# Optimization experiments

Measured on AMD Instinct MI355X. Metric: run time of the kernel, lower is better.

The kernel has to match this reference:

```python
import jax, jax.numpy as jnp
import numpy as np
from jax import lax

# problem sizes and solver hyperparameters
B, N, G, T = 8, 128, 100, 24
N_ITERS, LR, RHO = 40, 2e-4, 10.0
VOLL, VOSP = 1000.0, 50.0
RES_UP, RES_DN, RT_UP, RT_DN, RAMP_F = 0.05, 0.02, 2.0, 0.5, 1.0


def setup_inputs() -> dict:
    k = jax.random.split(jax.random.key(0), 8)
    pmin = jax.random.uniform(k[0], (G,), minval=10.0, maxval=50.0)
    pmax = pmin + jax.random.uniform(k[1], (G,), minval=100.0, maxval=300.0)
    b_G = jax.random.uniform(k[2], (G,), minval=10.0, maxval=40.0)
    c_G = jax.random.uniform(k[3], (G,), minval=0.0, maxval=5.0)
    lo, hi = pmin.sum(), pmax.sum()
    forecast = lo + jax.random.uniform(k[4], (B, T)) * 0.5 * (hi - lo)
    omega_scen = 0.05 * hi * jax.random.normal(k[5], (B, N, T))
    om_min = omega_scen.min(axis=1) - 1.0
    om_max = omega_scen.max(axis=1) + 1.0
    eps = jax.random.uniform(k[6], (B,)) * 5.0
    return dict(forecast=forecast, omega_scen=omega_scen, om_min=om_min,
                om_max=om_max, eps=eps, pmin=pmin, pmax=pmax, b_G=b_G, c_G=c_G)


def _solve_one(forecast, omega, om_min, om_max, eps, pmin, pmax, b, c):
    # forecast [T], omega [N,T], om_min/om_max [T], eps scalar
    ramp = pmax * RAMP_F
    rup_p, rdn_p = RES_UP * b, RES_DN * b
    rtu_p, rtd_p = RT_UP * b, RT_DN * b
    dist_max = (om_max[None, :] - omega).sum(-1)   # [N]
    dist_min = (omega - om_min[None, :]).sum(-1)   # [N]

    def objective(v):
        Cost = b[:, None] * v['P'] + c[:, None]
        stage1 = (Cost.sum() + (rup_p[:, None] * v['R_up']).sum()
                  + (rdn_p[:, None] * v['R_dn']).sum())
        Qn = (jnp.einsum('g,ngt->n', rtu_p, v['d_up'])
              + jnp.einsum('g,ngt->n', rtd_p, v['d_dn'])
              + VOLL * v['LS'].sum(-1) + VOSP * v['SP'].sum(-1))
        Qmax = ((rtu_p[:, None] * v['du_max']).sum() + (rtd_p[:, None] * v['dd_max']).sum()
                + VOLL * v['LS_max'].sum() + VOSP * v['SP_max'].sum())
        Qmin = ((rtu_p[:, None] * v['du_min']).sum() + (rtd_p[:, None] * v['dd_min']).sum()
                + VOLL * v['LS_min'].sum() + VOSP * v['SP_min'].sum())
        # epigraph phi[n] >= Qn, >= Qmax - gamma*dist_max, >= Qmin - gamma*dist_min
        phi = jnp.maximum(Qn, jnp.maximum(Qmax - v['gamma'] * dist_max,
                                          Qmin - v['gamma'] * dist_min))
        obj = stage1 + phi.mean() + eps * v['gamma']
        return obj, (phi, Cost)

    def penalty(v):
        relu = jax.nn.relu
        dP = v['P'][:, 1:] - v['P'][:, :-1]
        res = [
            # equality constraints
            v['P'].sum(0) - forecast,
            (v['d_up'] - v['d_dn']).sum(1) + v['LS'] - v['SP'] - omega,
            (v['du_max'] - v['dd_max']).sum(0) + v['LS_max'] - v['SP_max'] - om_max,
            (v['du_min'] - v['dd_min']).sum(0) + v['LS_min'] - v['SP_min'] - om_min,
            # inequality constraints (relu of violation)
            relu(v['P'] + v['R_up'] - pmax[:, None]),
            relu(pmin[:, None] - (v['P'] - v['R_dn'])),
            relu(v['d_up'] - v['R_up'][None]),
            relu(v['d_dn'] - v['R_dn'][None]),
            relu(v['du_max'] - v['R_up']), relu(v['dd_max'] - v['R_dn']),
            relu(v['du_min'] - v['R_up']), relu(v['dd_min'] - v['R_dn']),
            relu(jnp.abs(dP) - ramp[:, None]),
        ]
        total = jnp.zeros(())
        for r in res:
            total = total + (r * r).sum()
        return total

    def loss(v):
        return objective(v)[0] + RHO * penalty(v)

    def project(v):
        v = {kk: jnp.maximum(vv, 0.0) for kk, vv in v.items()}
        v['P'] = jnp.clip(v['P'], pmin[:, None], pmax[:, None])
        return v

    z_gt = jnp.zeros((G, T))
    v0 = {'P': jnp.broadcast_to(0.5 * (pmin + pmax)[:, None], (G, T)),
          'R_up': z_gt, 'R_dn': z_gt,
          'd_up': jnp.zeros((N, G, T)), 'd_dn': jnp.zeros((N, G, T)),
          'LS': jnp.zeros((N, T)), 'SP': jnp.zeros((N, T)),
          'du_max': z_gt, 'dd_max': z_gt,
          'LS_max': jnp.zeros((T,)), 'SP_max': jnp.zeros((T,)),
          'du_min': z_gt, 'dd_min': z_gt,
          'LS_min': jnp.zeros((T,)), 'SP_min': jnp.zeros((T,)),
          'gamma': jnp.zeros(())}
    grad_fn = jax.grad(loss)

    def step(v, _):
        g = grad_fn(v)
        v = jax.tree_util.tree_map(lambda x, gx: x - LR * gx, v, g)
        return project(v), None

    v, _ = lax.scan(step, v0, None, length=N_ITERS)
    obj, (phi, Cost) = objective(v)
    return v['P'], v['R_up'], v['R_dn'], Cost, phi, v['gamma'], obj


def reference(forecast, omega_scen, om_min, om_max, eps, pmin, pmax, b_G, c_G):
    solve = jax.vmap(_solve_one, in_axes=(0, 0, 0, 0, 0, None, None, None, None))
    P, R_up, R_dn, Cost, phi, gamma, obj = solve(
        forecast, omega_scen, om_min, om_max, eps, pmin, pmax, b_G, c_G)
    return P, R_up, R_dn, Cost, phi, gamma, obj
```

## Files before the change

### kernel.cpp

```cpp
#include <hip/hip_runtime.h>
#include <hip/hip_cooperative_groups.h>

namespace cg = cooperative_groups;

#define G_ 100
#define T_ 24
#define NSC 128
#define BATCH 8
#define NITER 40
#define NBLK (BATCH*T_)
#define NTHR 512
#define GMAX 13

typedef unsigned long long u64;

__device__ __forceinline__ u64 gload64(const u64* p){
  return __hip_atomic_load(p, __ATOMIC_RELAXED, __HIP_MEMORY_SCOPE_AGENT);
}
__device__ __forceinline__ void gstore64(u64* p, u64 v){
  __hip_atomic_store(p, v, __ATOMIC_RELAXED, __HIP_MEMORY_SCOPE_AGENT);
}
__device__ __forceinline__ u64 pack(float v, unsigned tag){
  return ((u64)tag<<32) | (u64)__float_as_uint(v);
}
__device__ __forceinline__ float unpackv(u64 x){ return __uint_as_float((unsigned)x); }
__device__ __forceinline__ unsigned unpackt(u64 x){ return (unsigned)(x>>32); }

__device__ __forceinline__ void blockReduce2(float& a, float& b, float* sR){
#pragma unroll
  for (int off=32; off; off>>=1){ a+=__shfl_down(a,off,64); b+=__shfl_down(b,off,64); }
  const int w = threadIdx.x>>6;
  __syncthreads();
  if ((threadIdx.x&63)==0){ sR[w]=a; sR[8+w]=b; }
  __syncthreads();
  a=0.f; b=0.f;
#pragma unroll
  for (int i=0;i<8;++i){ a+=sR[i]; b+=sR[8+i]; }
}

__global__ __launch_bounds__(NTHR, 1) void dro_kernel(
    const float* __restrict__ forecast, const float* __restrict__ omega,
    const float* __restrict__ om_min, const float* __restrict__ om_max,
    const float* __restrict__ eps_in, const float* __restrict__ pmin_g,
    const float* __restrict__ pmax_g, const float* __restrict__ bG,
    const float* __restrict__ cG, float* __restrict__ out, float* __restrict__ ws)
{
  constexpr float LR=2e-4f, VOLL=1000.f, VOSP=50.f, TWO_RHO=20.f, INVN=1.f/128.f;
  const int blk=blockIdx.x;
  const int b=blk&7;
  const int t_own=blk>>3;
  const int tid=threadIdx.x, wave=tid>>6, lane=tid&63;
  const int gcnt  = (wave<4)? 13 : 12;
  const int gbase = (wave<4)? wave*13 : 52+(wave-4)*12;

  __shared__ float sRu[G_], sRd[G_];
  __shared__ float sP[G_], sduM[G_], sddM[G_], sdum[G_], sddm[G_];
  __shared__ float sAccU[G_], sAccD[G_];
  __shared__ float sB[G_], sPmin[G_], sPmax[G_], sC[G_];
  __shared__ float sLS[NSC], sSP[NSC], sOm[NSC];
  __shared__ float sGQ[NSC], sR220[NSC];
  __shared__ float sQn[NSC], sDM[NSC], sDm[NSC], sS2[NSC];
  __shared__ float sQp[NSC*9], sSp[NSC*9];
  __shared__ float sQnP[NTHR];
  __shared__ float sRed[40];
  __shared__ float sScal[12];

  u64* W = (u64*)ws;
  u64* QNP = W;
  u64* PP  = W + 73728;
  u64* QS  = W + 147456;
  u64* GAM = W + 156672;
  u64* ST1 = W + 157056;

  const float epsv  = eps_in[b];
  const float omaxT = om_max[b*T_ + t_own];
  const float ominT = om_min[b*T_ + t_own];
  const float fctT  = forecast[b*T_ + t_own];

  float duA[GMAX], duB[GMAX], ddA[GMAX], ddB[GMAX];

  if (tid<G_){
    sB[tid]=bG[tid]; sPmin[tid]=pmin_g[tid]; sPmax[tid]=pmax_g[tid]; sC[tid]=cG[tid];
    sRu[tid]=0.f; sRd[tid]=0.f;
    sduM[tid]=0.f; sddM[tid]=0.f; sdum[tid]=0.f; sddm[tid]=0.f;
    sAccU[tid]=0.f; sAccD[tid]=0.f;
  }
  if (tid<NSC){
    const int n=tid;
    sLS[n]=0.f; sSP[n]=0.f; sS2[n]=0.f;
    sOm[n]=omega[(b*NSC+n)*T_+t_own];
    float dM=0.f,dm=0.f;
    for (int t=0;t<T_;++t){
      float o=omega[(b*NSC+n)*T_+t];
      dM+=om_max[b*T_+t]-o; dm+=o-om_min[b*T_+t];
    }
    sDM[n]=dM; sDm[n]=dm;
  }
  if (tid==0){ sScal[3]=0.f; sScal[4]=0.f; sScal[5]=0.f; sScal[6]=0.f; }
  __syncthreads();
#pragma unroll
  for (int j=0;j<GMAX;++j){ duA[j]=0.f; duB[j]=0.f; ddA[j]=0.f; ddB[j]=0.f; }
  {
    float p0=0.f;
    if (tid<G_){
      p0=0.5f*(sPmin[tid]+sPmax[tid]);
      sP[tid]=p0;
      gstore64(&PP[b*3072 + t_own*128 + tid], pack(p0,1u));
    }
    if (tid<NSC) gstore64(&QNP[b*3072 + t_own*128 + tid], pack(0.f,1u));
    if (tid<2)   gstore64(&QS[(b*T_ + t_own)*16 + tid], pack(0.f,1u));
    if (t_own==0 && tid==0) gstore64(&GAM[b*16], pack(0.f,1u));
    float rp=p0, dum0=0.f;
    blockReduce2(rp,dum0,sRed);
    if (tid==0){
      sScal[0]=-omaxT; sScal[1]=-ominT; sScal[2]=rp-fctT;
    }
  }
  __syncthreads();

  for (int k=0;k<=NITER;++k){
    const unsigned tg = (unsigned)(k+1);
    const int rb = k%3, wb = (k+1)%3;
    const u64* qnpR = QNP + rb*24576 + b*3072;
    const u64* ppR  = PP  + rb*24576 + b*3072;
    const u64* qsR  = QS  + (rb*BATCH + b)*T_*16;
    const u64* gamR = GAM + (rb*BATCH + b)*16;
    u64* qnpW = QNP + wb*24576 + b*3072 + t_own*128;
    u64* ppW  = PP  + wb*24576 + b*3072 + t_own*128;
    u64* qsW  = QS  + (wb*BATCH + b)*T_*16 + t_own*16;
    u64* gamW = GAM + (wb*BATCH + b)*16;

    const int n = tid&127, sb0 = (tid>>7)*6;
    u64 xq[6];
#pragma unroll
    for (int s=0;s<6;++s) xq[s]=gload64(&qnpR[(sb0+s)*128 + n]);
    u64 xm=0, xp=0;
    if (tid<G_){
      if (t_own>0)     xm = gload64(&ppR[(t_own-1)*128 + tid]);
      if (t_own<T_-1)  xp = gload64(&ppR[(t_own+1)*128 + tid]);
    }
    u64 xs0=0, xs1=0, xg=0;
    if (wave==0){
      if (lane<T_){ xs0=gload64(&qsR[lane*16]); xs1=gload64(&qsR[lane*16+1]); }
      xg=gload64(gamR);
    }
    for (;;){
      bool any=false;
#pragma unroll
      for (int s=0;s<6;++s)
        if (unpackt(xq[s])!=tg){ any=true; xq[s]=gload64(&qnpR[(sb0+s)*128 + n]); }
      if (!any) break;
      __builtin_amdgcn_s_sleep(1);
    }
    if (tid<G_){
      if (t_own>0)    while (unpackt(xm)!=tg){ __builtin_amdgcn_s_sleep(1); xm=gload64(&ppR[(t_own-1)*128 + tid]); }
      if (t_own<T_-1) while (unpackt(xp)!=tg){ __builtin_amdgcn_s_sleep(1); xp=gload64(&ppR[(t_own+1)*128 + tid]); }
    }
    float Qmax=0.f, Qmin=0.f, gamma=0.f;
    if (wave==0){
      if (lane<T_){
        while (unpackt(xs0)!=tg){ __builtin_amdgcn_s_sleep(1); xs0=gload64(&qsR[lane*16]); }
        while (unpackt(xs1)!=tg){ __builtin_amdgcn_s_sleep(1); xs1=gload64(&qsR[lane*16+1]); }
        Qmax=unpackv(xs0); Qmin=unpackv(xs1);
      }
      while (unpackt(xg)!=tg){ __builtin_amdgcn_s_sleep(1); xg=gload64(gamR); }
      gamma=unpackv(xg);
      if (lane==0) sScal[11]=gamma;
    }
    sQnP[tid]=unpackv(xq[0])+unpackv(xq[1])+unpackv(xq[2])
             +unpackv(xq[3])+unpackv(xq[4])+unpackv(xq[5]);
    const float pm1=unpackv(xm), pp1=unpackv(xp);
    __syncthreads();

    if (k==NITER){
      if (wave==0){
#pragma unroll
        for (int off=32; off; off>>=1){ Qmax+=__shfl_xor(Qmax,off,64); Qmin+=__shfl_xor(Qmin,off,64); }
        if (lane==0){ sScal[8]=Qmax; sScal[9]=Qmin; }
      }
      __syncthreads();
      const float Qm=sScal[8], Qn2=sScal[9], gam=sScal[11];
      if (tid<NSC){
        const float qsum=sQnP[tid]+sQnP[tid+128]+sQnP[tid+256]+sQnP[tid+384];
        const float ph=fmaxf(qsum,fmaxf(Qm-gam*sDM[tid],Qn2-gam*sDm[tid]));
        sQn[tid]=ph;
        if (t_own==0) out[76800 + b*NSC + tid]=ph;
      }
      float st=0.f, dum0=0.f;
      if (tid<G_){
        const int g=tid;
        const float Pv=sP[g];
        const float costv=sB[g]*Pv+sC[g];
        st=costv + 0.05f*sB[g]*sRu[g] + 0.02f*sB[g]*sRd[g];
        const int o=b*2400 + g*T_ + t_own;
        out[o]=Pv;
        out[19200+o]=sRu[g];
        out[38400+o]=sRd[g];
        out[57600+o]=costv;
      }
      blockReduce2(st,dum0,sRed);
      if (tid==0) gstore64(&ST1[(b*T_+t_own)*16], pack(st,99u));
      if (t_own==0){
        if (tid==0) out[77824+b]=gam;
        float s1=0.f;
        if (tid<64){
          u64 xs = (lane<T_)? gload64(&ST1[(b*T_+lane)*16]) : pack(0.f,99u);
          while (unpackt(xs)!=99u){ __builtin_amdgcn_s_sleep(1); xs=gload64(&ST1[(b*T_+lane)*16]); }
          s1=unpackv(xs);
        }
        float pm=(tid<NSC)? sQn[tid] : 0.f;
        blockReduce2(pm,s1,sRed);
        if (tid==0) out[77832+b] = s1 + pm*INVN + epsv*gam;
      }
      break;
    }

    if (wave==0){
#pragma unroll
      for (int off=32; off; off>>=1){ Qmax+=__shfl_xor(Qmax,off,64); Qmin+=__shfl_xor(Qmin,off,64); }
      float g1l=0.f,g2l=0.f,sgl=0.f;
#pragma unroll
      for (int h=0;h<2;++h){
        const int nn=lane+h*64;
        const float Qn=sQnP[nn]+sQnP[nn+128]+sQnP[nn+256]+sQnP[nn+384];
        const float m1=Qmax-gamma*sDM[nn], m2=Qmin-gamma*sDm[nn];
        const float inner=fmaxf(m1,m2), ph=fmaxf(Qn,inner);
        const float gQn=(Qn==ph?1.f:0.f)/((inner==ph)?2.f:1.f);
        const float gIn=(inner==ph?1.f:0.f)/((Qn==ph)?2.f:1.f);
        const float gm1=gIn*(m1==inner?1.f:0.f)/((m2==inner)?2.f:1.f);
        const float gm2=gIn*(m2==inner?1.f:0.f)/((m1==inner)?2.f:1.f);
        const float gq=gQn*INVN;
        sGQ[nn]=gq;
        g1l+=gm1; g2l+=gm2; sgl+=gm1*sDM[nn]+gm2*sDm[nn];
        const float r2=sS2[nn]+sLS[nn]-sSP[nn]-sOm[nn];
        const float r220=TWO_RHO*r2;
        sR220[nn]=r220;
        sLS[nn]=fmaxf(sLS[nn]-LR*(gq*VOLL+r220),0.f);
        sSP[nn]=fmaxf(sSP[nn]-LR*(gq*VOSP-r220),0.f);
      }
#pragma unroll
      for (int off=32; off; off>>=1){
        g1l+=__shfl_xor(g1l,off,64); g2l+=__shfl_xor(g2l,off,64); sgl+=__shfl_xor(sgl,off,64);
      }
      if (lane==0){ sScal[8]=g1l; sScal[9]=g2l; sScal[10]=sgl; }
    }
    __syncthreads();

    const float gqA=sGQ[lane],    r220A=sR220[lane];
    const float gqB=sGQ[lane+64], r220B=sR220[lane+64];
    float qvA=0.f,qvB=0.f,svA=0.f,svB=0.f;
#pragma unroll
    for (int j=0;j<GMAX;++j){
      if (j<gcnt){
        const int g=gbase+j;
        const float bg=sB[g];
        const float rtu=2.f*bg, rtd=0.5f*bg;
        const float ru=sRu[g], rd=sRd[g];
        const float r7A=fmaxf(duA[j]-ru,0.f), r8A=fmaxf(ddA[j]-rd,0.f);
        const float r7B=fmaxf(duB[j]-ru,0.f), r8B=fmaxf(ddB[j]-rd,0.f);
        duA[j]=fmaxf(duA[j]-LR*(gqA*rtu+(r220A+TWO_RHO*r7A)),0.f);
        ddA[j]=fmaxf(ddA[j]-LR*(gqA*rtd+(TWO_RHO*r8A-r220A)),0.f);
        duB[j]=fmaxf(duB[j]-LR*(gqB*rtu+(r220B+TWO_RHO*r7B)),0.f);
        ddB[j]=fmaxf(ddB[j]-LR*(gqB*rtd+(TWO_RHO*r8B-r220B)),0.f);
        qvA+=rtu*duA[j]+rtd*ddA[j];  svA+=duA[j]-ddA[j];
        qvB+=rtu*duB[j]+rtd*ddB[j];  svB+=duB[j]-ddB[j];
      }
    }
    sQp[lane*9+wave]=qvA;      sSp[lane*9+wave]=svA;
    sQp[(lane+64)*9+wave]=qvB; sSp[(lane+64)*9+wave]=svB;
    __syncthreads();

    const unsigned tg2 = (unsigned)(k+2);
    if (tid>=256 && tid<384){
      const int nn=tid-256;
      float q=0.f,s=0.f;
#pragma unroll
      for (int w=0;w<8;++w){ q+=sQp[nn*9+w]; s+=sSp[nn*9+w]; }
      sS2[nn]=s;
      q += VOLL*sLS[nn]+VOSP*sSP[nn];
      gstore64(&qnpW[nn], pack(q,tg2));
    }
    const float r3=sScal[0], r4=sScal[1], rP=sScal[2];
    const float S1s=sScal[8], S2s=sScal[9];
    float pQx=0.f,pQn2=0.f,pr3=0.f,pr4=0.f,pP=0.f;
    if (tid<G_){
      const int g=tid;
      const float rupS=sAccU[g], rdnS=sAccD[g];
      const float Pold=sP[g], ru=sRu[g], rd=sRd[g];
      const float duMo=sduM[g], ddMo=sddM[g], dumo=sdum[g], ddmo=sddm[g];
      const float r5 =fmaxf(Pold+ru-sPmax[g],0.f);
      const float r6 =fmaxf(sPmin[g]-Pold+rd,0.f);
      const float r9 =fmaxf(duMo-ru,0.f), r10=fmaxf(ddMo-rd,0.f);
      const float r11=fmaxf(dumo-ru,0.f), r12=fmaxf(ddmo-rd,0.f);
      const float rampg=sPmax[g];
      float gP=sB[g]+TWO_RHO*(rP+r5-r6);
      if (t_own>0){
        const float dp=Pold-pm1;
        gP+=TWO_RHO*fmaxf(fabsf(dp)-rampg,0.f)*(dp>=0.f?1.f:-1.f);
      }
      if (t_own<T_-1){
        const float dq=pp1-Pold;
        gP-=TWO_RHO*fmaxf(fabsf(dq)-rampg,0.f)*(dq>=0.f?1.f:-1.f);
      }
      const float Pn=fminf(fmaxf(Pold-LR*gP,sPmin[g]),sPmax[g]);
      sP[g]=Pn; gstore64(&ppW[g], pack(Pn,tg2));
      const float rtuB=2.f*sB[g], rtdB=0.5f*sB[g];
      sRu[g]=fmaxf(ru-LR*(0.05f*sB[g]+TWO_RHO*(r5-rupS-r9-r11)),0.f);
      sRd[g]=fmaxf(rd-LR*(0.02f*sB[g]+TWO_RHO*(r6-rdnS-r10-r12)),0.f);
      const float duMn=fmaxf(duMo-LR*(INVN*S1s*rtuB+TWO_RHO*( r3+r9 )),0.f);
      const float ddMn=fmaxf(ddMo-LR*(INVN*S1s*rtdB+TWO_RHO*(-r3+r10)),0.f);
      const float dumn=fmaxf(dumo-LR*(INVN*S2s*rtuB+TWO_RHO*( r4+r11)),0.f);
      const float ddmn=fmaxf(ddmo-LR*(INVN*S2s*rtdB+TWO_RHO*(-r4+r12)),0.f);
      sduM[g]=duMn; sddM[g]=ddMn; sdum[g]=dumn; sddm[g]=ddmn;
      pQx=rtuB*duMn+rtdB*ddMn; pQn2=rtuB*dumn+rtdB*ddmn;
      pr3=duMn-ddMn; pr4=dumn-ddmn; pP=Pn;
    }
    if (t_own==0 && tid==448)
      gstore64(gamW, pack(fmaxf(sScal[11]-LR*(epsv-INVN*sScal[10]),0.f), tg2));

#pragma unroll
    for (int off=32; off; off>>=1){
      pQx+=__shfl_down(pQx,off,64);  pQn2+=__shfl_down(pQn2,off,64);
      pr3+=__shfl_down(pr3,off,64);  pr4+=__shfl_down(pr4,off,64);
      pP +=__shfl_down(pP,off,64);
    }
    if (lane==0){
      sRed[wave]=pQx; sRed[8+wave]=pQn2; sRed[16+wave]=pr3;
      sRed[24+wave]=pr4; sRed[32+wave]=pP;
    }
    __syncthreads();

    if (tid==0){
      float aQx=0.f,aQn2=0.f,a3=0.f,a4=0.f,aP=0.f;
#pragma unroll
      for (int i=0;i<8;++i){
        aQx+=sRed[i]; aQn2+=sRed[8+i]; a3+=sRed[16+i]; a4+=sRed[24+i]; aP+=sRed[32+i];
      }
      const float LSMn=fmaxf(sScal[3]-LR*(INVN*S1s*VOLL+TWO_RHO*r3),0.f);
      const float SPMn=fmaxf(sScal[4]-LR*(INVN*S1s*VOSP-TWO_RHO*r3),0.f);
      const float LSmn=fmaxf(sScal[5]-LR*(INVN*S2s*VOLL+TWO_RHO*r4),0.f);
      const float SPmn=fmaxf(sScal[6]-LR*(INVN*S2s*VOSP-TWO_RHO*r4),0.f);
      sScal[3]=LSMn; sScal[4]=SPMn; sScal[5]=LSmn; sScal[6]=SPmn;
      gstore64(&qsW[0], pack(aQx + VOLL*LSMn + VOSP*SPMn, tg2));
      gstore64(&qsW[1], pack(aQn2 + VOLL*LSmn + VOSP*SPmn, tg2));
      sScal[0]=a3 + LSMn - SPMn - omaxT;
      sScal[1]=a4 + LSmn - SPmn - ominT;
      sScal[2]=aP - fctT;
    }

#pragma unroll
    for (int j=0;j<GMAX;++j){
      if (j<gcnt){
        const int g=gbase+j;
        const float ru=sRu[g], rd=sRd[g];
        float aU=fmaxf(duA[j]-ru,0.f)+fmaxf(duB[j]-ru,0.f);
        float aD=fmaxf(ddA[j]-rd,0.f)+fmaxf(ddB[j]-rd,0.f);
#pragma unroll
        for (int off=32; off; off>>=1){ aU+=__shfl_xor(aU,off,64); aD+=__shfl_xor(aD,off,64); }
        if (lane==0){ sAccU[g]=aU; sAccD[g]=aD; }
      }
    }
  }
}

extern "C" void kernel_launch(void* const* d_in, const int* in_sizes, int n_in,
                              void* d_out, int out_size, void* d_ws, size_t ws_size,
                              hipStream_t stream) {
  const float* forecast = (const float*)d_in[0];
  const float* omega    = (const float*)d_in[1];
  const float* omin     = (const float*)d_in[2];
  const float* omax     = (const float*)d_in[3];
  const float* eps      = (const float*)d_in[4];
  const float* pmin     = (const float*)d_in[5];
  const float* pmax     = (const float*)d_in[6];
  const float* bG       = (const float*)d_in[7];
  const float* cG       = (const float*)d_in[8];
  float* out = (float*)d_out;
  float* ws  = (float*)d_ws;
  void* args[] = { &forecast, &omega, &omin, &omax, &eps, &pmin, &pmax, &bG, &cG, &out, &ws };
  hipLaunchCooperativeKernel((const void*)dro_kernel, dim3(NBLK), dim3(NTHR),
                             args, 0, stream);
}
```

Baseline: 476.1 us.

## Move per-generator update into a single wave and cut block barriers

The per-generator P/R/dual update now runs in wave 1, two generators per lane. Its state lives in registers instead of shared memory, and the block-wide reduction is replaced by a single wave shuffle reduction. This removes one __syncthreads and the tid==0 serial reduction. The reserve accumulator reduction is folded into the earlier d_up/d_dn loop, the gamma update moves to the wave that owns the reduction, and all cross-block polls are merged into one spin loop. The cost is that a single wave now does more serial work per iteration, and correctness depends on the barrier ordering staying valid.

```diff
diff --git a/kernel.cpp b/kernel.cpp
--- a/kernel.cpp
+++ b/kernel.cpp
@@ -53,8 +53,7 @@
   const int gcnt  = (wave<4)? 13 : 12;
   const int gbase = (wave<4)? wave*13 : 52+(wave-4)*12;
 
-  __shared__ float sRu[G_], sRd[G_];
-  __shared__ float sP[G_], sduM[G_], sddM[G_], sdum[G_], sddm[G_];
+  __shared__ float sRu[G_], sRd[G_], sP[G_];
   __shared__ float sAccU[G_], sAccD[G_];
   __shared__ float sB[G_], sPmin[G_], sPmax[G_], sC[G_];
   __shared__ float sLS[NSC], sSP[NSC], sOm[NSC];
@@ -62,8 +61,8 @@
   __shared__ float sQn[NSC], sDM[NSC], sDm[NSC], sS2[NSC];
   __shared__ float sQp[NSC*9], sSp[NSC*9];
   __shared__ float sQnP[NTHR];
-  __shared__ float sRed[40];
-  __shared__ float sScal[12];
+  __shared__ float sRed[16];
+  __shared__ float sScal[6];
 
   u64* W = (u64*)ws;
   u64* QNP = W;
@@ -78,25 +77,25 @@
   const float fctT  = forecast[b*T_ + t_own];
 
   float duA[GMAX], duB[GMAX], ddA[GMAX], ddB[GMAX];
+  float duMr[2]={0.f,0.f}, ddMr[2]={0.f,0.f}, dumr[2]={0.f,0.f}, ddmr[2]={0.f,0.f};
+  float lsm=0.f, spm=0.f, lsn=0.f, spn=0.f;
+  float r3reg=0.f, r4reg=0.f, rPreg=0.f;
 
   if (tid<G_){
     sB[tid]=bG[tid]; sPmin[tid]=pmin_g[tid]; sPmax[tid]=pmax_g[tid]; sC[tid]=cG[tid];
     sRu[tid]=0.f; sRd[tid]=0.f;
-    sduM[tid]=0.f; sddM[tid]=0.f; sdum[tid]=0.f; sddm[tid]=0.f;
-    sAccU[tid]=0.f; sAccD[tid]=0.f;
   }
   if (tid<NSC){
-    const int n=tid;
-    sLS[n]=0.f; sSP[n]=0.f; sS2[n]=0.f;
-    sOm[n]=omega[(b*NSC+n)*T_+t_own];
+    const int nn=tid;
+    sLS[nn]=0.f; sSP[nn]=0.f; sS2[nn]=0.f;
+    sOm[nn]=omega[(b*NSC+nn)*T_+t_own];
     float dM=0.f,dm=0.f;
     for (int t=0;t<T_;++t){
-      float o=omega[(b*NSC+n)*T_+t];
+      float o=omega[(b*NSC+nn)*T_+t];
       dM+=om_max[b*T_+t]-o; dm+=o-om_min[b*T_+t];
     }
-    sDM[n]=dM; sDm[n]=dm;
+    sDM[nn]=dM; sDm[nn]=dm;
   }
-  if (tid==0){ sScal[3]=0.f; sScal[4]=0.f; sScal[5]=0.f; sScal[6]=0.f; }
   __syncthreads();
 #pragma unroll
   for (int j=0;j<GMAX;++j){ duA[j]=0.f; duB[j]=0.f; ddA[j]=0.f; ddB[j]=0.f; }
@@ -112,14 +111,13 @@
     if (t_own==0 && tid==0) gstore64(&GAM[b*16], pack(0.f,1u));
     float rp=p0, dum0=0.f;
     blockReduce2(rp,dum0,sRed);
-    if (tid==0){
-      sScal[0]=-omaxT; sScal[1]=-ominT; sScal[2]=rp-fctT;
-    }
+    r3reg=-omaxT; r4reg=-ominT; rPreg=rp-fctT;
   }
   __syncthreads();
 
   for (int k=0;k<=NITER;++k){
-    const unsigned tg = (unsigned)(k+1);
+    const unsigned tg  = (unsigned)(k+1);
+    const unsigned tg2 = (unsigned)(k+2);
     const int rb = k%3, wb = (k+1)%3;
     const u64* qnpR = QNP + rb*24576 + b*3072;
     const u64* ppR  = PP  + rb*24576 + b*3072;
@@ -131,55 +129,49 @@
     u64* gamW = GAM + (wb*BATCH + b)*16;
 
     const int n = tid&127, sb0 = (tid>>7)*6;
-    u64 xq[6];
-#pragma unroll
-    for (int s=0;s<6;++s) xq[s]=gload64(&qnpR[(sb0+s)*128 + n]);
-    u64 xm=0, xp=0;
-    if (tid<G_){
-      if (t_own>0)     xm = gload64(&ppR[(t_own-1)*128 + tid]);
-      if (t_own<T_-1)  xp = gload64(&ppR[(t_own+1)*128 + tid]);
-    }
-    u64 xs0=0, xs1=0, xg=0;
-    if (wave==0){
-      if (lane<T_){ xs0=gload64(&qsR[lane*16]); xs1=gload64(&qsR[lane*16+1]); }
-      xg=gload64(gamR);
-    }
+    const bool w1 = (wave==1), hasG1 = w1 && (lane<36);
+    u64 xq[6]; 
+#pragma unroll
+    for (int s=0;s<6;++s) xq[s]=0ull;
+    u64 xm0=0,xp0=0,xm1=0,xp1=0,xs0=0,xs1=0,xg=0;
     for (;;){
-      bool any=false;
+      bool pend=false;
 #pragma unroll
       for (int s=0;s<6;++s)
-        if (unpackt(xq[s])!=tg){ any=true; xq[s]=gload64(&qnpR[(sb0+s)*128 + n]); }
-      if (!any) break;
+        if (unpackt(xq[s])!=tg){ xq[s]=gload64(&qnpR[(sb0+s)*128+n]); pend=true; }
+      if (w1){
+        if (t_own>0){
+          if (unpackt(xm0)!=tg){ xm0=gload64(&ppR[(t_own-1)*128+lane]); pend=true; }
+          if (hasG1 && unpackt(xm1)!=tg){ xm1=gload64(&ppR[(t_own-1)*128+lane+64]); pend=true; }
+        }
+        if (t_own<T_-1){
+          if (unpackt(xp0)!=tg){ xp0=gload64(&ppR[(t_own+1)*128+lane]); pend=true; }
+          if (hasG1 && unpackt(xp1)!=tg){ xp1=gload64(&ppR[(t_own+1)*128+lane+64]); pend=true; }
+        }
+      } else if (wave==0){
+        if (lane<T_){
+          if (unpackt(xs0)!=tg){ xs0=gload64(&qsR[lane*16]);   pend=true; }
+          if (unpackt(xs1)!=tg){ xs1=gload64(&qsR[lane*16+1]); pend=true; }
+        }
+        if (unpackt(xg)!=tg){ xg=gload64(gamR); pend=true; }
+      }
+      if (!pend) break;
       __builtin_amdgcn_s_sleep(1);
-    }
-    if (tid<G_){
-      if (t_own>0)    while (unpackt(xm)!=tg){ __builtin_amdgcn_s_sleep(1); xm=gload64(&ppR[(t_own-1)*128 + tid]); }
-      if (t_own<T_-1) while (unpackt(xp)!=tg){ __builtin_amdgcn_s_sleep(1); xp=gload64(&ppR[(t_own+1)*128 + tid]); }
-    }
-    float Qmax=0.f, Qmin=0.f, gamma=0.f;
-    if (wave==0){
-      if (lane<T_){
-        while (unpackt(xs0)!=tg){ __builtin_amdgcn_s_sleep(1); xs0=gload64(&qsR[lane*16]); }
-        while (unpackt(xs1)!=tg){ __builtin_amdgcn_s_sleep(1); xs1=gload64(&qsR[lane*16+1]); }
-        Qmax=unpackv(xs0); Qmin=unpackv(xs1);
-      }
-      while (unpackt(xg)!=tg){ __builtin_amdgcn_s_sleep(1); xg=gload64(gamR); }
-      gamma=unpackv(xg);
-      if (lane==0) sScal[11]=gamma;
     }
     sQnP[tid]=unpackv(xq[0])+unpackv(xq[1])+unpackv(xq[2])
              +unpackv(xq[3])+unpackv(xq[4])+unpackv(xq[5]);
-    const float pm1=unpackv(xm), pp1=unpackv(xp);
+    float Qmax=unpackv(xs0), Qmin=unpackv(xs1);
+    const float gamma=unpackv(xg);
     __syncthreads();
 
     if (k==NITER){
       if (wave==0){
 #pragma unroll
         for (int off=32; off; off>>=1){ Qmax+=__shfl_xor(Qmax,off,64); Qmin+=__shfl_xor(Qmin,off,64); }
-        if (lane==0){ sScal[8]=Qmax; sScal[9]=Qmin; }
+        if (lane==0){ sScal[2]=Qmax; sScal[3]=Qmin; sScal[4]=gamma; }
       }
       __syncthreads();
-      const float Qm=sScal[8], Qn2=sScal[9], gam=sScal[11];
+      const float Qm=sScal[2], Qn2=sScal[3], gam=sScal[4];
       if (tid<NSC){
         const float qsum=sQnP[tid]+sQnP[tid+128]+sQnP[tid+256]+sQnP[tid+384];
         const float ph=fmaxf(qsum,fmaxf(Qm-gam*sDM[tid],Qn2-gam*sDm[tid]));
@@ -242,7 +234,9 @@
       for (int off=32; off; off>>=1){
         g1l+=__shfl_xor(g1l,off,64); g2l+=__shfl_xor(g2l,off,64); sgl+=__shfl_xor(sgl,off,64);
       }
-      if (lane==0){ sScal[8]=g1l; sScal[9]=g2l; sScal[10]=sgl; }
+      if (lane==0){ sScal[0]=g1l; sScal[1]=g2l; }
+      if (t_own==0 && lane==0)
+        gstore64(gamW, pack(fmaxf(gamma-LR*(epsv-INVN*sgl),0.f), tg2));
     }
     __syncthreads();
 
@@ -258,6 +252,10 @@
         const float ru=sRu[g], rd=sRd[g];
         const float r7A=fmaxf(duA[j]-ru,0.f), r8A=fmaxf(ddA[j]-rd,0.f);
         const float r7B=fmaxf(duB[j]-ru,0.f), r8B=fmaxf(ddB[j]-rd,0.f);
+        float aU=r7A+r7B, aD=r8A+r8B;
+#pragma unroll
+        for (int off=32; off; off>>=1){ aU+=__shfl_xor(aU,off,64); aD+=__shfl_xor(aD,off,64); }
+        if (lane==0){ sAccU[g]=aU; sAccD[g]=aD; }
         duA[j]=fmaxf(duA[j]-LR*(gqA*rtu+(r220A+TWO_RHO*r7A)),0.f);
         ddA[j]=fmaxf(ddA[j]-LR*(gqA*rtd+(TWO_RHO*r8A-r220A)),0.f);
         duB[j]=fmaxf(duB[j]-LR*(gqB*rtu+(r220B+TWO_RHO*r7B)),0.f);
@@ -270,94 +268,70 @@
     sQp[(lane+64)*9+wave]=qvB; sSp[(lane+64)*9+wave]=svB;
     __syncthreads();
 
-    const unsigned tg2 = (unsigned)(k+2);
-    if (tid>=256 && tid<384){
-      const int nn=tid-256;
+    if (tid>=128 && tid<256){
+      const int nn=tid-128;
       float q=0.f,s=0.f;
 #pragma unroll
       for (int w=0;w<8;++w){ q+=sQp[nn*9+w]; s+=sSp[nn*9+w]; }
       sS2[nn]=s;
       q += VOLL*sLS[nn]+VOSP*sSP[nn];
       gstore64(&qnpW[nn], pack(q,tg2));
-    }
-    const float r3=sScal[0], r4=sScal[1], rP=sScal[2];
-    const float S1s=sScal[8], S2s=sScal[9];
-    float pQx=0.f,pQn2=0.f,pr3=0.f,pr4=0.f,pP=0.f;
-    if (tid<G_){
-      const int g=tid;
-      const float rupS=sAccU[g], rdnS=sAccD[g];
-      const float Pold=sP[g], ru=sRu[g], rd=sRd[g];
-      const float duMo=sduM[g], ddMo=sddM[g], dumo=sdum[g], ddmo=sddm[g];
-      const float r5 =fmaxf(Pold+ru-sPmax[g],0.f);
-      const float r6 =fmaxf(sPmin[g]-Pold+rd,0.f);
-      const float r9 =fmaxf(duMo-ru,0.f), r10=fmaxf(ddMo-rd,0.f);
-      const float r11=fmaxf(dumo-ru,0.f), r12=fmaxf(ddmo-rd,0.f);
-      const float rampg=sPmax[g];
-      float gP=sB[g]+TWO_RHO*(rP+r5-r6);
-      if (t_own>0){
-        const float dp=Pold-pm1;
-        gP+=TWO_RHO*fmaxf(fabsf(dp)-rampg,0.f)*(dp>=0.f?1.f:-1.f);
-      }
-      if (t_own<T_-1){
-        const float dq=pp1-Pold;
-        gP-=TWO_RHO*fmaxf(fabsf(dq)-rampg,0.f)*(dq>=0.f?1.f:-1.f);
-      }
-      const float Pn=fminf(fmaxf(Pold-LR*gP,sPmin[g]),sPmax[g]);
-      sP[g]=Pn; gstore64(&ppW[g], pack(Pn,tg2));
-      const float rtuB=2.f*sB[g], rtdB=0.5f*sB[g];
-      sRu[g]=fmaxf(ru-LR*(0.05f*sB[g]+TWO_RHO*(r5-rupS-r9-r11)),0.f);
-      sRd[g]=fmaxf(rd-LR*(0.02f*sB[g]+TWO_RHO*(r6-rdnS-r10-r12)),0.f);
-      const float duMn=fmaxf(duMo-LR*(INVN*S1s*rtuB+TWO_RHO*( r3+r9 )),0.f);
-      const float ddMn=fmaxf(ddMo-LR*(INVN*S1s*rtdB+TWO_RHO*(-r3+r10)),0.f);
-      const float dumn=fmaxf(dumo-LR*(INVN*S2s*rtuB+TWO_RHO*( r4+r11)),0.f);
-      const float ddmn=fmaxf(ddmo-LR*(INVN*S2s*rtdB+TWO_RHO*(-r4+r12)),0.f);
-      sduM[g]=duMn; sddM[g]=ddMn; sdum[g]=dumn; sddm[g]=ddmn;
-      pQx=rtuB*duMn+rtdB*ddMn; pQn2=rtuB*dumn+rtdB*ddmn;
-      pr3=duMn-ddMn; pr4=dumn-ddmn; pP=Pn;
-    }
-    if (t_own==0 && tid==448)
-      gstore64(gamW, pack(fmaxf(sScal[11]-LR*(epsv-INVN*sScal[10]),0.f), tg2));
-
-#pragma unroll
-    for (int off=32; off; off>>=1){
-      pQx+=__shfl_down(pQx,off,64);  pQn2+=__shfl_down(pQn2,off,64);
-      pr3+=__shfl_down(pr3,off,64);  pr4+=__shfl_down(pr4,off,64);
-      pP +=__shfl_down(pP,off,64);
-    }
-    if (lane==0){
-      sRed[wave]=pQx; sRed[8+wave]=pQn2; sRed[16+wave]=pr3;
-      sRed[24+wave]=pr4; sRed[32+wave]=pP;
-    }
-    __syncthreads();
-
-    if (tid==0){
-      float aQx=0.f,aQn2=0.f,a3=0.f,a4=0.f,aP=0.f;
-#pragma unroll
-      for (int i=0;i<8;++i){
-        aQx+=sRed[i]; aQn2+=sRed[8+i]; a3+=sRed[16+i]; a4+=sRed[24+i]; aP+=sRed[32+i];
-      }
-      const float LSMn=fmaxf(sScal[3]-LR*(INVN*S1s*VOLL+TWO_RHO*r3),0.f);
-      const float SPMn=fmaxf(sScal[4]-LR*(INVN*S1s*VOSP-TWO_RHO*r3),0.f);
-      const float LSmn=fmaxf(sScal[5]-LR*(INVN*S2s*VOLL+TWO_RHO*r4),0.f);
-      const float SPmn=fmaxf(sScal[6]-LR*(INVN*S2s*VOSP-TWO_RHO*r4),0.f);
-      sScal[3]=LSMn; sScal[4]=SPMn; sScal[5]=LSmn; sScal[6]=SPmn;
-      gstore64(&qsW[0], pack(aQx + VOLL*LSMn + VOSP*SPMn, tg2));
-      gstore64(&qsW[1], pack(aQn2 + VOLL*LSmn + VOSP*SPmn, tg2));
-      sScal[0]=a3 + LSMn - SPMn - omaxT;
-      sScal[1]=a4 + LSmn - SPmn - ominT;
-      sScal[2]=aP - fctT;
-    }
-
-#pragma unroll
-    for (int j=0;j<GMAX;++j){
-      if (j<gcnt){
-        const int g=gbase+j;
-        const float ru=sRu[g], rd=sRd[g];
-        float aU=fmaxf(duA[j]-ru,0.f)+fmaxf(duB[j]-ru,0.f);
-        float aD=fmaxf(ddA[j]-rd,0.f)+fmaxf(ddB[j]-rd,0.f);
-#pragma unroll
-        for (int off=32; off; off>>=1){ aU+=__shfl_xor(aU,off,64); aD+=__shfl_xor(aD,off,64); }
-        if (lane==0){ sAccU[g]=aU; sAccD[g]=aD; }
+    } else if (w1){
+      const float r3=__shfl(r3reg,0,64), r4=__shfl(r4reg,0,64), rP=__shfl(rPreg,0,64);
+      const float S1s=sScal[0], S2s=sScal[1];
+      float pQx=0.f,pQn2=0.f,pr3=0.f,pr4=0.f,pP=0.f;
+#pragma unroll
+      for (int i=0;i<2;++i){
+        if (i==0 || hasG1){
+          const int g = lane + i*64;
+          const float rupS=sAccU[g], rdnS=sAccD[g];
+          const float Pold=sP[g], ru=sRu[g], rd=sRd[g];
+          const float duMo=duMr[i], ddMo=ddMr[i], dumo=dumr[i], ddmo=ddmr[i];
+          const float r5 =fmaxf(Pold+ru-sPmax[g],0.f);
+          const float r6 =fmaxf(sPmin[g]-Pold+rd,0.f);
+          const float r9 =fmaxf(duMo-ru,0.f), r10=fmaxf(ddMo-rd,0.f);
+          const float r11=fmaxf(dumo-ru,0.f), r12=fmaxf(ddmo-rd,0.f);
+          const float rampg=sPmax[g];
+          float gP=sB[g]+TWO_RHO*(rP+r5-r6);
+          if (t_own>0){
+            const float dp=Pold-unpackv(i==0?xm0:xm1);
+            gP+=TWO_RHO*fmaxf(fabsf(dp)-rampg,0.f)*(dp>=0.f?1.f:-1.f);
+          }
+          if (t_own<T_-1){
+            const float dq=unpackv(i==0?xp0:xp1)-Pold;
+            gP-=TWO_RHO*fmaxf(fabsf(dq)-rampg,0.f)*(dq>=0.f?1.f:-1.f);
+          }
+          const float Pn=fminf(fmaxf(Pold-LR*gP,sPmin[g]),sPmax[g]);
+          sP[g]=Pn; gstore64(&ppW[g], pack(Pn,tg2));
+          const float rtuB=2.f*sB[g], rtdB=0.5f*sB[g];
+          sRu[g]=fmaxf(ru-LR*(0.05f*sB[g]+TWO_RHO*(r5-rupS-r9-r11)),0.f);
+          sRd[g]=fmaxf(rd-LR*(0.02f*sB[g]+TWO_RHO*(r6-rdnS-r10-r12)),0.f);
+          const float duMn=fmaxf(duMo-LR*(INVN*S1s*rtuB+TWO_RHO*( r3+r9 )),0.f);
+          const float ddMn=fmaxf(ddMo-LR*(INVN*S1s*rtdB+TWO_RHO*(-r3+r10)),0.f);
+          const float dumn=fmaxf(dumo-LR*(INVN*S2s*rtuB+TWO_RHO*( r4+r11)),0.f);
+          const float ddmn=fmaxf(ddmo-LR*(INVN*S2s*rtdB+TWO_RHO*(-r4+r12)),0.f);
+          duMr[i]=duMn; ddMr[i]=ddMn; dumr[i]=dumn; ddmr[i]=ddmn;
+          pQx+=rtuB*duMn+rtdB*ddMn; pQn2+=rtuB*dumn+rtdB*ddmn;
+          pr3+=duMn-ddMn; pr4+=dumn-ddmn; pP+=Pn;
+        }
+      }
+#pragma unroll
+      for (int off=32; off; off>>=1){
+        pQx+=__shfl_down(pQx,off,64);  pQn2+=__shfl_down(pQn2,off,64);
+        pr3+=__shfl_down(pr3,off,64);  pr4+=__shfl_down(pr4,off,64);
+        pP +=__shfl_down(pP,off,64);
+      }
+      if (lane==0){
+        const float LSMn=fmaxf(lsm-LR*(INVN*S1s*VOLL+TWO_RHO*r3),0.f);
+        const float SPMn=fmaxf(spm-LR*(INVN*S1s*VOSP-TWO_RHO*r3),0.f);
+        const float LSmn=fmaxf(lsn-LR*(INVN*S2s*VOLL+TWO_RHO*r4),0.f);
+        const float SPmn=fmaxf(spn-LR*(INVN*S2s*VOSP-TWO_RHO*r4),0.f);
+        lsm=LSMn; spm=SPMn; lsn=LSmn; spn=SPmn;
+        gstore64(&qsW[0], pack(pQx + VOLL*LSMn + VOSP*SPMn, tg2));
+        gstore64(&qsW[1], pack(pQn2 + VOLL*LSmn + VOSP*SPmn, tg2));
+        r3reg=pr3 + LSMn - SPMn - omaxT;
+        r4reg=pr4 + LSmn - SPmn - ominT;
+        rPreg=pP - fctT;
       }
     }
   }
```

Result: slower. 605.4 us (+27.1%).
